# Performance work log

Hardware: AMD Instinct MI355X
Metric: run time of the kernel (lower is better)

## Reference

```python
import jax, jax.numpy as jnp
import numpy as np

VOXEL_SIZE = 0.05  # init kwarg


def setup_inputs() -> dict:
    key = jax.random.key(0)
    N, B = 4_194_304, 16
    # coords uniform in [0, 5)^3 -> ~100^3 voxel cells per scene at voxel_size=0.05
    coord = jax.random.uniform(key, (N, 3), dtype=jnp.float32) * 5.0
    # cumulative batch offsets (equal-sized scenes), as pointops expects
    offset = (jnp.arange(1, B + 1, dtype=jnp.int32) * (N // B)).astype(jnp.int32)
    return {"coord": coord, "offset": offset}


def _voxel_mean(coord, offset, voxel_size):
    """Faithful jax port of voxelize_helper + segment_csr(mean) + batch2offset.

    Returns:
      n_p    [N,3]  voxel-mean coords, padded with zeros beyond n_voxels
      n_o    [B]    cumulative voxel counts per batch (batch2offset)
      counts [N]    points per voxel (idx_ptr = concat([0], cumsum(counts[valid])))
    """
    N = coord.shape[0]
    B = offset.shape[0]
    # batch id per point from cumulative offsets
    batch = jnp.searchsorted(offset, jnp.arange(N), side='right')  # [N]
    # start = per-batch min coord (start=None path of voxelize_helper)
    start = jax.ops.segment_min(coord, batch, num_segments=B)      # [B,3]
    grid = jnp.floor((coord - start[batch]) / voxel_size).astype(jnp.int32)  # [N,3]
    G = jnp.max(grid) + 1  # grid extent (per-axis upper bound)
    # linearized cluster key: unique per (batch, gx, gy, gz)
    ckey = ((batch * G + grid[:, 0]) * G + grid[:, 1]) * G + grid[:, 2]
    fill = B * G * G * G  # sentinel beyond any real key
    # sorted unique cluster keys == CSR segment order after sorting cluster indices
    uniq, inv = jnp.unique(ckey, return_inverse=True, size=N, fill_value=fill)
    # fused gather + segment-mean (equivalent to coord[sorted_idx] -> segment_csr mean)
    seg_sum = jax.ops.segment_sum(coord, inv, num_segments=N)                 # [N,3]
    counts = jax.ops.segment_sum(jnp.ones((N,), coord.dtype), inv, num_segments=N)
    n_p = seg_sum / jnp.maximum(counts, 1.0)[:, None]
    # batch id per voxel -> batch2offset (cumulative voxel counts)
    valid = uniq < fill
    vbatch = jnp.where(valid, uniq // (G * G * G), B)
    per_batch = jax.ops.segment_sum(valid.astype(jnp.int32), vbatch, num_segments=B + 1)[:B]
    n_o = jnp.cumsum(per_batch)
    return n_p, n_o, counts.astype(jnp.int32)


def reference(coord, offset):
    return _voxel_mean(coord, offset, VOXEL_SIZE)
```

## Files before the change

kernel.cpp:

```cpp
#include <hip/hip_runtime.h>
#include <stdint.h>


typedef unsigned int uint;
typedef unsigned short u16;
typedef unsigned long long u64;

#define VS 0.05f
#define QSCALE (4096.0f / VS)
#define QINV  (VS / 4096.0f)
#define NBUCKET 2048
#define NBLK_P 256
#define DENSE_MAX 4096

__device__ __forceinline__ uint f2m(float f) {
    uint b = __float_as_uint(f);
    return (b & 0x80000000u) ? ~b : (b | 0x80000000u);
}
__device__ __forceinline__ float m2f(uint m) {
    uint b = (m & 0x80000000u) ? (m & 0x7fffffffu) : ~m;
    return __uint_as_float(b);
}

__global__ void k_init(uint* start_m, int B3) {
    int i = blockIdx.x * blockDim.x + threadIdx.x;
    if (i < B3) start_m[i] = 0xFFFFFFFFu;
}

__global__ void __launch_bounds__(256)
k_minmax(const float* __restrict__ coord, const int* __restrict__ offset,
         int N, int B, uint* start_m) {
    __shared__ uint smin[768];
    __shared__ int soff[256];
    int t = threadIdx.x;
    int nb3 = B * 3;
    for (int j = t; j < B; j += 256) soff[j] = offset[j];
    for (int j = t; j < nb3; j += 256) smin[j] = 0xFFFFFFFFu;
    __syncthreads();

    int F = 3 * N;
    int NQ = F >> 2;
    int per = (NQ + gridDim.x - 1) / gridDim.x;
    int qlo = blockIdx.x * per;
    int qhi = min(NQ, qlo + per);
    const float4* __restrict__ c4 = reinterpret_cast<const float4*>(coord);

    bool fast = false;
    int bU = 0;
    if (qlo < qhi) {
        int pF = (4 * qlo) / 3;
        int pL = (4 * qhi - 1) / 3;
        int bF = 0, bL = 0;
        for (int j = 0; j < B; ++j) {
            bF += (pF >= soff[j]) ? 1 : 0;
            bL += (pL >= soff[j]) ? 1 : 0;
        }
        fast = (bF == bL);
        bU = bF;
    }

    if (fast) {
        int q = qlo + t;
        int p0 = q % 3;
        float s0 = INFINITY, s1 = INFINITY, s2 = INFINITY;
        for (;;) {
            if (q >= qhi) break;
            float4 v = c4[q];
            s0 = fminf(s0, fminf(v.x, v.w)); s1 = fminf(s1, v.y); s2 = fminf(s2, v.z);
            q += 256;
            if (q >= qhi) break;
            v = c4[q];
            s1 = fminf(s1, fminf(v.x, v.w)); s2 = fminf(s2, v.y); s0 = fminf(s0, v.z);
            q += 256;
            if (q >= qhi) break;
            v = c4[q];
            s2 = fminf(s2, fminf(v.x, v.w)); s0 = fminf(s0, v.y); s1 = fminf(s1, v.z);
            q += 256;
        }
        float ax, ay, az;
        if (p0 == 0)      { ax = s0; ay = s1; az = s2; }
        else if (p0 == 1) { ax = s2; ay = s0; az = s1; }
        else              { ax = s1; ay = s2; az = s0; }
        for (int d = 32; d; d >>= 1) {
            ax = fminf(ax, __shfl_xor(ax, d));
            ay = fminf(ay, __shfl_xor(ay, d));
            az = fminf(az, __shfl_xor(az, d));
        }
        if ((t & 63) == 0 && ax < INFINITY) {
            atomicMin(&smin[bU * 3 + 0], f2m(ax));
            atomicMin(&smin[bU * 3 + 1], f2m(ay));
            atomicMin(&smin[bU * 3 + 2], f2m(az));
        }
    } else {
        for (int q = qlo + t; q < qhi; q += 256) {
            float4 v = c4[q];
            int e = 4 * q;
            float vals[4] = {v.x, v.y, v.z, v.w};
#pragma unroll
            for (int k = 0; k < 4; ++k) {
                int ee = e + k;
                int pt = ee / 3;
                int axis = ee - 3 * pt;
                int b = 0;
                for (int j = 0; j < B; ++j) b += (pt >= soff[j]) ? 1 : 0;
                atomicMin(&smin[b * 3 + axis], f2m(vals[k]));
            }
        }
    }

    if (blockIdx.x == 0) {
        for (int ee = 4 * NQ + t; ee < F; ee += 256) {
            int pt = ee / 3;
            int axis = ee - 3 * pt;
            int b = 0;
            for (int j = 0; j < B; ++j) b += (pt >= soff[j]) ? 1 : 0;
            atomicMin(&smin[b * 3 + axis], f2m(coord[ee]));
        }
    }
    __syncthreads();
    for (int j = t; j < nb3; j += 256) {
        uint mn = smin[j];
        if (mn != 0xFFFFFFFFu) atomicMin(&start_m[j], mn);
    }
}


__device__ __forceinline__ u64 mk_rec(float x, float y, float z,
                                      float sx, float sy, float sz,
                                      int b, uint& q) {
    int gx = min((int)floorf((x - sx) / VS), 127);
    int gy = min((int)floorf((y - sy) / VS), 127);
    int gz = min((int)floorf((z - sz) / VS), 127);
    float fx = fmaxf(x - (sx + (float)gx * VS), 0.0f);
    float fy = fmaxf(y - (sy + (float)gy * VS), 0.0f);
    float fz = fmaxf(z - (sz + (float)gz * VS), 0.0f);
    uint ux = min((uint)(fx * QSCALE + 0.5f), 4095u);
    uint uy = min((uint)(fy * QSCALE + 0.5f), 4095u);
    uint uz = min((uint)(fz * QSCALE + 0.5f), 4095u);
    uint cell = ((uint)gy << 7) | (uint)gz;
    q = ((uint)b << 7) | (uint)gx;
    return ((u64)q << 50) | ((u64)cell << 36) | ((u64)ux << 24) | ((u64)uy << 12) | (u64)uz;
}

__device__ __forceinline__ void count_point(float x, float y, float z, int b,
                                            float sx, float sy, float sz, int pid,
                                            uint* hist, u64* __restrict__ tmp) {
    uint q;
    u64 rec = mk_rec(x, y, z, sx, sy, sz, b, q);
    atomicAdd(&hist[q], 1u);
    tmp[pid] = rec;
}

__global__ void __launch_bounds__(1024)
k_count3(const float* __restrict__ coord, const int* __restrict__ offset,
         int N, int B, const uint* __restrict__ start_m, uint* __restrict__ histm,
         u64* __restrict__ tmp) {
    __shared__ uint hist[NBUCKET];
    __shared__ int soff[16];
    __shared__ float sstart[48];
    int t = threadIdx.x;
    if (t < B) soff[t] = offset[t];
    if (t < B * 3) sstart[t] = m2f(start_m[t]);
    for (int j = t; j < NBUCKET; j += 1024) hist[j] = 0;
    __syncthreads();
    int chunk = (N + gridDim.x - 1) / gridDim.x;
    int lo = blockIdx.x * chunk, hi = min(N, lo + chunk);
    int bLo = 0, bHi = 0;
    for (int j = 0; j < B; ++j) {
        bLo += (lo >= soff[j]) ? 1 : 0;
        bHi += (hi - 1 >= soff[j]) ? 1 : 0;
    }
    if (lo < hi && bLo == bHi && (lo & 3) == 0) {
        int b = bLo;
        float sx = sstart[b * 3 + 0], sy = sstart[b * 3 + 1], sz = sstart[b * 3 + 2];
        const float4* __restrict__ c4 = reinterpret_cast<const float4*>(coord);
        int gEnd = hi >> 2;
        for (int g = (lo >> 2) + t; g < gEnd; g += 1024) {
            float4 v0 = c4[3 * g], v1 = c4[3 * g + 1], v2 = c4[3 * g + 2];
            int p = 4 * g;
            count_point(v0.x, v0.y, v0.z, b, sx, sy, sz, p + 0, hist, tmp);
            count_point(v0.w, v1.x, v1.y, b, sx, sy, sz, p + 1, hist, tmp);
            count_point(v1.z, v1.w, v2.x, b, sx, sy, sz, p + 2, hist, tmp);
            count_point(v2.y, v2.z, v2.w, b, sx, sy, sz, p + 3, hist, tmp);
        }
        for (int i = (gEnd << 2) + t; i < hi; i += 1024) {
            float x = coord[3 * i + 0], y = coord[3 * i + 1], z = coord[3 * i + 2];
            count_point(x, y, z, b, sx, sy, sz, i, hist, tmp);
        }
    } else {
        for (int i = lo + t; i < hi; i += 1024) {
            float x = coord[3 * i + 0], y = coord[3 * i + 1], z = coord[3 * i + 2];
            int b = 0;
            for (int j = 0; j < B; ++j) b += (i >= soff[j]) ? 1 : 0;
            count_point(x, y, z, b, sstart[b * 3 + 0], sstart[b * 3 + 1],
                        sstart[b * 3 + 2], i, hist, tmp);
        }
    }
    __syncthreads();
    for (int j = t; j < NBUCKET; j += 1024)
        histm[(size_t)j * NBLK_P + blockIdx.x] = hist[j];
}

__global__ void __launch_bounds__(256)
k_scanrow(uint* __restrict__ histm, uint* __restrict__ tot) {
    __shared__ uint wtot[4], woff[4];
    uint* row = histm + (size_t)blockIdx.x * NBLK_P;
    int t = threadIdx.x;
    uint v = row[t];
    uint sc = v;
    for (int d = 1; d < 64; d <<= 1) {
        uint nb = __shfl_up(sc, d, 64);
        if ((t & 63) >= d) sc += nb;
    }
    if ((t & 63) == 63) wtot[t >> 6] = sc;
    __syncthreads();
    if (t == 0) {
        uint r = 0;
#pragma unroll
        for (int k = 0; k < 4; ++k) { woff[k] = r; r += wtot[k]; }
    }
    __syncthreads();
    uint incl = sc + woff[t >> 6];
    row[t] = incl - v;
    if (t == 255) tot[blockIdx.x] = incl;
}

__global__ void __launch_bounds__(1024)
k_scan2048(const uint* __restrict__ in, uint* __restrict__ out) {
    __shared__ uint wtot[16], woff[16];
    int t = threadIdx.x;
    uint a = in[2 * t], bb = in[2 * t + 1];
    uint s = a + bb;
    uint sc = s;
    for (int d = 1; d < 64; d <<= 1) {
        uint nb = __shfl_up(sc, d, 64);
        if ((t & 63) >= d) sc += nb;
    }
    if ((t & 63) == 63) wtot[t >> 6] = sc;
    __syncthreads();
    if (t == 0) {
        uint r = 0;
#pragma unroll
        for (int k = 0; k < 16; ++k) { woff[k] = r; r += wtot[k]; }
    }
    __syncthreads();
    uint incl = sc + woff[t >> 6];
    uint ex = incl - s;
    out[2 * t] = ex;
    out[2 * t + 1] = ex + a;
    if (t == 1023) out[2048] = incl;
}

__global__ void __launch_bounds__(1024)
k_scan2048b(const uint* __restrict__ in, uint* __restrict__ out,
            int B, float* __restrict__ no_out) {
    __shared__ uint wtot[16], woff[16];
    int t = threadIdx.x;
    uint a = in[2 * t], bb = in[2 * t + 1];
    uint s = a + bb;
    uint sc = s;
    for (int d = 1; d < 64; d <<= 1) {
        uint nb = __shfl_up(sc, d, 64);
        if ((t & 63) >= d) sc += nb;
    }
    if ((t & 63) == 63) wtot[t >> 6] = sc;
    __syncthreads();
    if (t == 0) {
        uint r = 0;
#pragma unroll
        for (int k = 0; k < 16; ++k) { woff[k] = r; r += wtot[k]; }
    }
    __syncthreads();
    uint incl = sc + woff[t >> 6];
    uint ex = incl - s;
    out[2 * t] = ex;
    out[2 * t + 1] = ex + a;
    if (t == 1023) out[2048] = incl;
    int tp = t + 1;
    if ((tp & 63) == 0) {
        int b = (tp >> 6) - 1;
        if (b < B) no_out[b] = (float)incl;
    }
}

__global__ void __launch_bounds__(1024)
k_scatter(const u64* __restrict__ tmp, int N,
          const uint* __restrict__ histm, const uint* __restrict__ bucket_base,
          u64* __restrict__ recs) {
    __shared__ uint cursor[NBUCKET];
    int t = threadIdx.x;
    for (int j = t; j < NBUCKET; j += 1024)
        cursor[j] = bucket_base[j] + histm[(size_t)j * NBLK_P + blockIdx.x];
    __syncthreads();
    int chunk = (N + gridDim.x - 1) / gridDim.x;
    int lo = blockIdx.x * chunk, hi = min(N, lo + chunk);
    for (int i = lo + t; i < hi; i += 1024) {
        u64 r = tmp[i];
        uint q = (uint)(r >> 50);
        uint slot = atomicAdd(&cursor[q], 1u);
        recs[slot] = r;
    }
}

__global__ void __launch_bounds__(256)
k_vox(const u64* __restrict__ recs, const uint* __restrict__ bucket_base,
      uint* __restrict__ voxcount, uint* __restrict__ gmask) {
    __shared__ uint bits[512];
    __shared__ uint wsum[4];
    int q = blockIdx.x;
    int t = threadIdx.x;
    uint lo = bucket_base[q], hi = bucket_base[q + 1];
    bits[t] = 0;
    bits[t + 256] = 0;
    __syncthreads();
    for (uint i = lo + t; i < hi; i += 256) {
        uint c = (uint)(recs[i] >> 36) & 0x3FFFu;
        atomicOr(&bits[c >> 5], 1u << (c & 31));
    }
    __syncthreads();
    uint m0 = bits[t], m1 = bits[t + 256];
    gmask[(size_t)q * 512 + t] = m0;
    gmask[(size_t)q * 512 + t + 256] = m1;
    uint s = __popc(m0) + __popc(m1);
    for (int d = 32; d; d >>= 1) s += __shfl_xor(s, d);
    if ((t & 63) == 0) wsum[t >> 6] = s;
    __syncthreads();
    if (t == 0) voxcount[q] = wsum[0] + wsum[1] + wsum[2] + wsum[3];
}

__global__ void __launch_bounds__(1024)
k_emit2(const u64* __restrict__ recs, const uint* __restrict__ bucket_base,
        const uint* __restrict__ voxscan, const uint* __restrict__ gmask,
        const uint* __restrict__ start_m, int N, int B, int out_total,
        float* __restrict__ np_out, float* __restrict__ cnt_out,
        float* __restrict__ out) {
    int t = threadIdx.x;
    if (blockIdx.x >= NBUCKET) {
        uint total = voxscan[NBUCKET];
        int zb = blockIdx.x - NBUCKET;
        int stride = (gridDim.x - NBUCKET) * 1024;
        int tid = zb * 1024 + t;
        for (int j = 3 * (int)total + tid; j < 3 * N; j += stride) np_out[j] = 0.0f;
        for (int j = (int)total + tid; j < N; j += stride) cnt_out[j] = 0.0f;
        for (int j = 4 * N + B + tid; j < out_total; j += stride) out[j] = 0.0f;
        return;
    }
    __shared__ u64 dense[DENSE_MAX];
    __shared__ uint mask[512], wrank[512];
    __shared__ u16 cellOf[DENSE_MAX];
    __shared__ uint wtot[8], woff[9];
    __shared__ float sstart[48];
    int q = blockIdx.x;
    uint lo = bucket_base[q], hi = bucket_base[q + 1];
    if (lo == hi) return;
    if (t < 48) sstart[t] = m2f(start_m[t]);
    uint m = 0, c = 0;
    if (t < 512) {
        m = gmask[(size_t)q * 512 + t];
        mask[t] = m;
        c = __popc(m);
    }
    uint sc = c;
    for (int d = 1; d < 64; d <<= 1) {
        uint nb = __shfl_up(sc, d, 64);
        if ((t & 63) >= d) sc += nb;
    }
    if (t < 512 && (t & 63) == 63) wtot[t >> 6] = sc;
    __syncthreads();
    if (t == 0) {
        uint r = 0;
        for (int k = 0; k < 8; ++k) { woff[k] = r; r += wtot[k]; }
        woff[8] = r;
    }
    __syncthreads();
    uint myrank = sc - c + ((t < 512) ? woff[t >> 6] : 0);
    if (t < 512) wrank[t] = myrank;
    uint vc = woff[8];
    uint base_r = voxscan[q];
    int b = q >> 7, gx = q & 127;
    float cx = sstart[b * 3 + 0] + (float)gx * VS;
    float sy = sstart[b * 3 + 1], sz = sstart[b * 3 + 2];
    for (uint segbase = 0; segbase < vc; segbase += DENSE_MAX) {
        uint seglen = min(vc - segbase, (uint)DENSE_MAX);
        for (uint j = t; j < seglen; j += 1024) dense[j] = 0ull;
        if (t < 512) {
            uint mm = m;
            uint r = myrank;
            uint kbase = (uint)t << 5;
            while (mm) {
                uint bit = (uint)__ffs(mm) - 1u;
                mm &= mm - 1u;
                if (r >= segbase && r < segbase + seglen)
                    cellOf[r - segbase] = (u16)(kbase + bit);
                ++r;
            }
        }
        __syncthreads();
        for (uint i = lo + t; i < hi; i += 1024) {
            u64 rec = recs[i];
            uint cc = (uint)(rec >> 36) & 0x3FFFu;
            uint w = cc >> 5, bit = cc & 31;
            uint r = wrank[w] + __popc(mask[w] & ((1u << bit) - 1u));
            if (r >= segbase && r < segbase + seglen) {
                u64 enc = (((rec >> 24) & 0xFFFull) << 46) | (((rec >> 12) & 0xFFFull) << 28)
                        | ((rec & 0xFFFull) << 10) | 1ull;
                atomicAdd(&dense[r - segbase], enc);
            }
        }
        __syncthreads();
        for (uint rr = segbase + t; rr < segbase + seglen; rr += 1024) {
            uint cell = cellOf[rr - segbase];
            uint gy = cell >> 7, gz = cell & 127u;
            u64 p = dense[rr - segbase];
            float cnt = (float)(uint)(p & 1023ull);
            float inv = 1.0f / fmaxf(cnt, 1.0f);
            uint uz = (uint)((p >> 10) & 0x3FFFFull);
            uint uy = (uint)((p >> 28) & 0x3FFFFull);
            uint ux = (uint)(p >> 46);
            uint r_out = base_r + rr;
            np_out[3 * r_out + 0] = cx + ((float)ux * QINV) * inv;
            np_out[3 * r_out + 1] = sy + (float)gy * VS + ((float)uy * QINV) * inv;
            np_out[3 * r_out + 2] = sz + (float)gz * VS + ((float)uz * QINV) * inv;
            cnt_out[r_out] = cnt;
        }
        __syncthreads();
    }
}


__device__ __forceinline__ void point_grid(const float* __restrict__ coord, int i,
                                           const int* soff, const float* sstart, int B,
                                           float& x, float& y, float& z,
                                           int& b, int& gx, int& gy, int& gz) {
    x = coord[3 * i + 0]; y = coord[3 * i + 1]; z = coord[3 * i + 2];
    b = 0;
    for (int j = 0; j < B; ++j) b += (i >= soff[j]) ? 1 : 0;
    gx = min((int)floorf((x - sstart[b * 3 + 0]) / VS), 127);
    gy = min((int)floorf((y - sstart[b * 3 + 1]) / VS), 127);
    gz = min((int)floorf((z - sstart[b * 3 + 2]) / VS), 127);
}

__device__ __forceinline__ u64 frac12(float x, float y, float z,
                                      const float* sstart, int b,
                                      int gx, int gy, int gz) {
    float fx = fmaxf(x - (sstart[b * 3 + 0] + (float)gx * VS), 0.0f);
    float fy = fmaxf(y - (sstart[b * 3 + 1] + (float)gy * VS), 0.0f);
    float fz = fmaxf(z - (sstart[b * 3 + 2] + (float)gz * VS), 0.0f);
    uint ux = min((uint)(fx * QSCALE + 0.5f), 4095u);
    uint uy = min((uint)(fy * QSCALE + 0.5f), 4095u);
    uint uz = min((uint)(fz * QSCALE + 0.5f), 4095u);
    return ((u64)ux << 24) | ((u64)uy << 12) | (u64)uz;
}

__global__ void k_hist(const float* __restrict__ coord, const int* __restrict__ offset,
                       int N, int B, const uint* __restrict__ start_m,
                       uint* __restrict__ mask) {
    __shared__ int soff[256];
    __shared__ float sstart[768];
    for (int j = threadIdx.x; j < B; j += blockDim.x) soff[j] = offset[j];
    for (int j = threadIdx.x; j < B * 3; j += blockDim.x) sstart[j] = m2f(start_m[j]);
    __syncthreads();
    int i = blockIdx.x * blockDim.x + threadIdx.x;
    if (i >= N) return;
    float x, y, z; int b, gx, gy, gz;
    point_grid(coord, i, soff, sstart, B, x, y, z, b, gx, gy, gz);
    uint key = ((uint)b << 21) | ((uint)gx << 14) | ((uint)gy << 7) | (uint)gz;
    atomicOr(&mask[key >> 5], 1u << (key & 31));
}

__global__ void k_scan1(const uint* __restrict__ mask, uint* __restrict__ partial) {
    int base = blockIdx.x * 1024 + threadIdx.x * 4;
    uint4 m = *(const uint4*)(mask + base);
    uint s = __popc(m.x) + __popc(m.y) + __popc(m.z) + __popc(m.w);
    for (int d = 32; d; d >>= 1) s += __shfl_xor(s, d);
    __shared__ uint wsum[4];
    if ((threadIdx.x & 63) == 0) wsum[threadIdx.x >> 6] = s;
    __syncthreads();
    if (threadIdx.x == 0) partial[blockIdx.x] = wsum[0] + wsum[1] + wsum[2] + wsum[3];
}

__global__ void k_scan2(uint* partial, int P, uint* total) {
    __shared__ uint t[256];
    uint carry = 0;
    for (int base = 0; base < P; base += 256) {
        int j = base + threadIdx.x;
        uint v = (j < P) ? partial[j] : 0;
        t[threadIdx.x] = v;
        __syncthreads();
        for (int d = 1; d < 256; d <<= 1) {
            uint add = (threadIdx.x >= d) ? t[threadIdx.x - d] : 0;
            __syncthreads();
            t[threadIdx.x] += add;
            __syncthreads();
        }
        uint inc = t[threadIdx.x];
        uint chunk = t[255];
        if (j < P) partial[j] = carry + inc - v;
        __syncthreads();
        carry += chunk;
    }
    if (threadIdx.x == 0) *total = carry;
}

__global__ void k_scan3(const uint* __restrict__ mask, const uint* __restrict__ partial,
                        uint* __restrict__ wordrank) {
    int base = blockIdx.x * 1024 + threadIdx.x * 4;
    uint4 m = *(const uint4*)(mask + base);
    uint c0 = __popc(m.x), c1 = __popc(m.y), c2 = __popc(m.z), c3 = __popc(m.w);
    uint s = c0 + c1 + c2 + c3;
    __shared__ uint t[256];
    t[threadIdx.x] = s;
    __syncthreads();
    for (int d = 1; d < 256; d <<= 1) {
        uint add = (threadIdx.x >= d) ? t[threadIdx.x - d] : 0;
        __syncthreads();
        t[threadIdx.x] += add;
        __syncthreads();
    }
    uint ex = t[threadIdx.x] - s + partial[blockIdx.x];
    uint4 r;
    r.x = ex; r.y = ex + c0; r.z = ex + c0 + c1; r.w = ex + c0 + c1 + c2;
    *(uint4*)(wordrank + base) = r;
}

__global__ void k_no(const uint* mask, const uint* wordrank, const uint* total,
                     float* no_out, int B, int W) {
    int b = blockIdx.x * blockDim.x + threadIdx.x;
    if (b >= B) return;
    long long idx = (long long)(b + 1) << 21;
    uint w = (uint)(idx >> 5);
    uint v;
    if (w >= (uint)W) v = *total;
    else v = wordrank[w];
    no_out[b] = (float)v;
}

__global__ void k_accum_sparse(const float* __restrict__ coord, const int* __restrict__ offset,
                               int N, int B, const uint* __restrict__ start_m,
                               const uint* __restrict__ mask, const uint* __restrict__ wordrank,
                               u64* __restrict__ packed) {
    __shared__ int soff[256];
    __shared__ float sstart[768];
    for (int j = threadIdx.x; j < B; j += blockDim.x) soff[j] = offset[j];
    for (int j = threadIdx.x; j < B * 3; j += blockDim.x) sstart[j] = m2f(start_m[j]);
    __syncthreads();
    int i = blockIdx.x * blockDim.x + threadIdx.x;
    if (i >= N) return;
    float x, y, z; int b, gx, gy, gz;
    point_grid(coord, i, soff, sstart, B, x, y, z, b, gx, gy, gz);
    uint key = ((uint)b << 21) | ((uint)gx << 14) | ((uint)gy << 7) | (uint)gz;
    uint w = key >> 5, bit = key & 31;
    uint r = wordrank[w] + __popc(mask[w] & ((1u << bit) - 1u));
    u64 f = frac12(x, y, z, sstart, b, gx, gy, gz);
    u64 enc = (((f >> 24) & 0xFFFull) << 46) | (((f >> 12) & 0xFFFull) << 28)
            | ((f & 0xFFFull) << 10) | 1ull;
    atomicAdd(&packed[r], enc);
}

__global__ void k_decode_sparse(const uint* __restrict__ mask, const uint* __restrict__ wordrank,
                                const uint* __restrict__ start_m,
                                const u64* __restrict__ packed, int W,
                                float* __restrict__ np_out, float* __restrict__ cnt_out) {
    __shared__ float sstart[48];
    for (int j = threadIdx.x; j < 48; j += blockDim.x) sstart[j] = m2f(start_m[j]);
    __syncthreads();
    int w = blockIdx.x * blockDim.x + threadIdx.x;
    if (w >= W) return;
    uint m = mask[w];
    if (m == 0) return;
    uint r = wordrank[w];
    uint kbase = (uint)w << 5;
    while (m) {
        uint bit = (uint)__ffs(m) - 1u;
        m &= m - 1u;
        uint key = kbase + bit;
        u64 p = packed[r];
        float cnt = (float)(uint)(p & 1023ull);
        float inv = 1.0f / fmaxf(cnt, 1.0f);
        uint uz = (uint)((p >> 10) & 0x3FFFFull);
        uint uy = (uint)((p >> 28) & 0x3FFFFull);
        uint ux = (uint)(p >> 46);
        uint b = key >> 21;
        uint gx = (key >> 14) & 127u;
        uint gy = (key >> 7) & 127u;
        uint gz = key & 127u;
        np_out[3 * r + 0] = sstart[b * 3 + 0] + (float)gx * VS + ((float)ux * QINV) * inv;
        np_out[3 * r + 1] = sstart[b * 3 + 1] + (float)gy * VS + ((float)uy * QINV) * inv;
        np_out[3 * r + 2] = sstart[b * 3 + 2] + (float)gz * VS + ((float)uz * QINV) * inv;
        cnt_out[r] = cnt;
        ++r;
    }
}

extern "C" void kernel_launch(void* const* d_in, const int* in_sizes, int n_in,
                              void* d_out, int out_size, void* d_ws, size_t ws_size,
                              hipStream_t stream) {
    const float* coord = (const float*)d_in[0];
    const int* offset = (const int*)d_in[1];
    int N = in_sizes[0] / 3;
    int B = in_sizes[1];

    float* out = (float*)d_out;
    float* np_out = out;
    float* no_out = out + (size_t)3 * N;
    float* cnt_out = no_out + B;

    uint8_t* base = (uint8_t*)d_ws;
    uint* start_m = (uint*)base;
    uint* total = start_m + (size_t)B * 3;

    uintptr_t p = (uintptr_t)(total + 1);
    p = (p + 255) & ~(uintptr_t)255;
    uint* histm = (uint*)p;          p += (size_t)NBUCKET * NBLK_P * 4;
    p = (p + 255) & ~(uintptr_t)255;
    uint* tot = (uint*)p;            p += (size_t)NBUCKET * 4;
    p = (p + 255) & ~(uintptr_t)255;
    uint* bucket_base = (uint*)p;    p += (size_t)(NBUCKET + 1) * 4;
    p = (p + 255) & ~(uintptr_t)255;
    uint* voxcount = (uint*)p;       p += (size_t)NBUCKET * 4;
    p = (p + 255) & ~(uintptr_t)255;
    uint* voxscan = (uint*)p;        p += (size_t)(NBUCKET + 1) * 4;
    p = (p + 255) & ~(uintptr_t)255;
    uint* gmask = (uint*)p;          p += (size_t)NBUCKET * 512 * 4;
    p = (p + 255) & ~(uintptr_t)255;
    u64* recs = (u64*)p;             p += (size_t)N * 8;
    p = (p + 255) & ~(uintptr_t)255;
    u64* tmp = (u64*)p;              p += (size_t)N * 8;
    size_t need_part = p - (uintptr_t)base;

    k_init<<<(B * 3 + 255) / 256, 256, 0, stream>>>(start_m, B * 3);
    k_minmax<<<2048, 256, 0, stream>>>(coord, offset, N, B, start_m);

    if (B <= 16 && ws_size >= need_part) {
        k_count3<<<NBLK_P, 1024, 0, stream>>>(coord, offset, N, B, start_m, histm, tmp);
        k_scanrow<<<NBUCKET, 256, 0, stream>>>(histm, tot);
        k_scan2048<<<1, 1024, 0, stream>>>(tot, bucket_base);
        k_scatter<<<NBLK_P, 1024, 0, stream>>>(tmp, N, histm, bucket_base, recs);
        k_vox<<<NBUCKET, 256, 0, stream>>>(recs, bucket_base, voxcount, gmask);
        k_scan2048b<<<1, 1024, 0, stream>>>(voxcount, voxscan, B, no_out);
        k_emit2<<<NBUCKET + 1024, 1024, 0, stream>>>(recs, bucket_base, voxscan, gmask,
                                                     start_m, N, B, out_size,
                                                     np_out, cnt_out, out);
    } else {
        hipMemsetAsync(d_out, 0, (size_t)out_size * sizeof(float), stream);
        size_t W = (size_t)B << 16;
        int nblk1 = (int)(W / 1024);
        uintptr_t sp = (uintptr_t)(total + 1);
        sp = (sp + 255) & ~(uintptr_t)255;
        uint* partial = (uint*)sp;   sp += (size_t)nblk1 * 4;
        sp = (sp + 255) & ~(uintptr_t)255;
        uint* mask = (uint*)sp;      sp += W * 4;
        sp = (sp + 255) & ~(uintptr_t)255;
        uint* wordrank = (uint*)sp;  sp += W * 4;
        sp = (sp + 255) & ~(uintptr_t)255;
        u64* packed = (u64*)sp;
        int nb = (N + 255) / 256;
        hipMemsetAsync(mask, 0, W * sizeof(uint), stream);
        hipMemsetAsync(packed, 0, (size_t)N * sizeof(u64), stream);
        k_hist<<<nb, 256, 0, stream>>>(coord, offset, N, B, start_m, mask);
        k_scan1<<<nblk1, 256, 0, stream>>>(mask, partial);
        k_scan2<<<1, 256, 0, stream>>>(partial, nblk1, total);
        k_scan3<<<nblk1, 256, 0, stream>>>(mask, partial, wordrank);
        k_no<<<(B + 63) / 64, 64, 0, stream>>>(mask, wordrank, total, no_out, B, (int)W);
        k_accum_sparse<<<nb, 256, 0, stream>>>(coord, offset, N, B, start_m, mask,
                                               wordrank, packed);
        k_decode_sparse<<<(int)((W + 255) / 256), 256, 0, stream>>>(mask, wordrank, start_m,
                                                                    packed, (int)W,
                                                                    np_out, cnt_out);
    }
}
```

Measured before the change: 194.1 us.

## Fuse voxel accumulation into bitmap kernel, emit from compact per-bucket results

The per-bucket voxel accumulation (rank computation, shared-memory atomic sums, cell bookkeeping) moves from the emit kernel into the bitmap kernel. That kernel now writes packed sums and cell ids into bucket-local scratch slots, reusing the tmp buffer. The emit kernel only reads these compact results and writes outputs. This removes the second pass over all point records and the global bitmask round-trip. In exchange, the bitmap kernel does more work with 256 threads per block, which may lower parallelism and occupancy per bucket because of the larger shared memory.

```diff
diff --git a/kernel.cpp b/kernel.cpp
--- a/kernel.cpp
+++ b/kernel.cpp
@@ -303,10 +303,15 @@
 }
 
 __global__ void __launch_bounds__(256)
-k_vox(const u64* __restrict__ recs, const uint* __restrict__ bucket_base,
-      uint* __restrict__ voxcount, uint* __restrict__ gmask) {
+k_vox2(const u64* __restrict__ recs, const uint* __restrict__ bucket_base,
+       uint* __restrict__ voxcount, u64* __restrict__ packedv,
+       u16* __restrict__ cellv) {
     __shared__ uint bits[512];
-    __shared__ uint wsum[4];
+    __shared__ uint wrank[512];
+    __shared__ u64 dense[DENSE_MAX];
+    __shared__ u16 cellOf[DENSE_MAX];
+    __shared__ uint wtot[4], woff[4];
+    __shared__ uint shvc;
     int q = blockIdx.x;
     int t = threadIdx.x;
     uint lo = bucket_base[q], hi = bucket_base[q + 1];
@@ -318,75 +323,35 @@
         atomicOr(&bits[c >> 5], 1u << (c & 31));
     }
     __syncthreads();
-    uint m0 = bits[t], m1 = bits[t + 256];
-    gmask[(size_t)q * 512 + t] = m0;
-    gmask[(size_t)q * 512 + t + 256] = m1;
-    uint s = __popc(m0) + __popc(m1);
-    for (int d = 32; d; d >>= 1) s += __shfl_xor(s, d);
-    if ((t & 63) == 0) wsum[t >> 6] = s;
-    __syncthreads();
-    if (t == 0) voxcount[q] = wsum[0] + wsum[1] + wsum[2] + wsum[3];
-}
-
-__global__ void __launch_bounds__(1024)
-k_emit2(const u64* __restrict__ recs, const uint* __restrict__ bucket_base,
-        const uint* __restrict__ voxscan, const uint* __restrict__ gmask,
-        const uint* __restrict__ start_m, int N, int B, int out_total,
-        float* __restrict__ np_out, float* __restrict__ cnt_out,
-        float* __restrict__ out) {
-    int t = threadIdx.x;
-    if (blockIdx.x >= NBUCKET) {
-        uint total = voxscan[NBUCKET];
-        int zb = blockIdx.x - NBUCKET;
-        int stride = (gridDim.x - NBUCKET) * 1024;
-        int tid = zb * 1024 + t;
-        for (int j = 3 * (int)total + tid; j < 3 * N; j += stride) np_out[j] = 0.0f;
-        for (int j = (int)total + tid; j < N; j += stride) cnt_out[j] = 0.0f;
-        for (int j = 4 * N + B + tid; j < out_total; j += stride) out[j] = 0.0f;
-        return;
-    }
-    __shared__ u64 dense[DENSE_MAX];
-    __shared__ uint mask[512], wrank[512];
-    __shared__ u16 cellOf[DENSE_MAX];
-    __shared__ uint wtot[8], woff[9];
-    __shared__ float sstart[48];
-    int q = blockIdx.x;
-    uint lo = bucket_base[q], hi = bucket_base[q + 1];
-    if (lo == hi) return;
-    if (t < 48) sstart[t] = m2f(start_m[t]);
-    uint m = 0, c = 0;
-    if (t < 512) {
-        m = gmask[(size_t)q * 512 + t];
-        mask[t] = m;
-        c = __popc(m);
-    }
-    uint sc = c;
+    uint m0 = bits[2 * t], m1 = bits[2 * t + 1];
+    uint c0 = __popc(m0), c1 = __popc(m1);
+    uint s = c0 + c1;
+    uint sc = s;
     for (int d = 1; d < 64; d <<= 1) {
         uint nb = __shfl_up(sc, d, 64);
         if ((t & 63) >= d) sc += nb;
     }
-    if (t < 512 && (t & 63) == 63) wtot[t >> 6] = sc;
+    if ((t & 63) == 63) wtot[t >> 6] = sc;
     __syncthreads();
     if (t == 0) {
         uint r = 0;
-        for (int k = 0; k < 8; ++k) { woff[k] = r; r += wtot[k]; }
-        woff[8] = r;
-    }
-    __syncthreads();
-    uint myrank = sc - c + ((t < 512) ? woff[t >> 6] : 0);
-    if (t < 512) wrank[t] = myrank;
-    uint vc = woff[8];
-    uint base_r = voxscan[q];
-    int b = q >> 7, gx = q & 127;
-    float cx = sstart[b * 3 + 0] + (float)gx * VS;
-    float sy = sstart[b * 3 + 1], sz = sstart[b * 3 + 2];
+#pragma unroll
+        for (int k = 0; k < 4; ++k) { woff[k] = r; r += wtot[k]; }
+        shvc = r;
+        voxcount[q] = r;
+    }
+    __syncthreads();
+    uint ex = sc + woff[t >> 6] - s;
+    wrank[2 * t] = ex;
+    wrank[2 * t + 1] = ex + c0;
+    uint vc = shvc;
+    uint myr0 = ex;
+    uint myr1 = ex + c0;
     for (uint segbase = 0; segbase < vc; segbase += DENSE_MAX) {
         uint seglen = min(vc - segbase, (uint)DENSE_MAX);
-        for (uint j = t; j < seglen; j += 1024) dense[j] = 0ull;
-        if (t < 512) {
-            uint mm = m;
-            uint r = myrank;
-            uint kbase = (uint)t << 5;
+        for (uint j = t; j < seglen; j += 256) dense[j] = 0ull;
+        {
+            uint mm = m0, r = myr0, kbase = (uint)(2 * t) << 5;
             while (mm) {
                 uint bit = (uint)__ffs(mm) - 1u;
                 mm &= mm - 1u;
@@ -394,13 +359,21 @@
                     cellOf[r - segbase] = (u16)(kbase + bit);
                 ++r;
             }
+            mm = m1; r = myr1; kbase = (uint)(2 * t + 1) << 5;
+            while (mm) {
+                uint bit = (uint)__ffs(mm) - 1u;
+                mm &= mm - 1u;
+                if (r >= segbase && r < segbase + seglen)
+                    cellOf[r - segbase] = (u16)(kbase + bit);
+                ++r;
+            }
         }
         __syncthreads();
-        for (uint i = lo + t; i < hi; i += 1024) {
+        for (uint i = lo + t; i < hi; i += 256) {
             u64 rec = recs[i];
             uint cc = (uint)(rec >> 36) & 0x3FFFu;
             uint w = cc >> 5, bit = cc & 31;
-            uint r = wrank[w] + __popc(mask[w] & ((1u << bit) - 1u));
+            uint r = wrank[w] + __popc(bits[w] & ((1u << bit) - 1u));
             if (r >= segbase && r < segbase + seglen) {
                 u64 enc = (((rec >> 24) & 0xFFFull) << 46) | (((rec >> 12) & 0xFFFull) << 28)
                         | ((rec & 0xFFFull) << 10) | 1ull;
@@ -408,22 +381,56 @@
             }
         }
         __syncthreads();
-        for (uint rr = segbase + t; rr < segbase + seglen; rr += 1024) {
-            uint cell = cellOf[rr - segbase];
-            uint gy = cell >> 7, gz = cell & 127u;
-            u64 p = dense[rr - segbase];
-            float cnt = (float)(uint)(p & 1023ull);
-            float inv = 1.0f / fmaxf(cnt, 1.0f);
-            uint uz = (uint)((p >> 10) & 0x3FFFFull);
-            uint uy = (uint)((p >> 28) & 0x3FFFFull);
-            uint ux = (uint)(p >> 46);
-            uint r_out = base_r + rr;
-            np_out[3 * r_out + 0] = cx + ((float)ux * QINV) * inv;
-            np_out[3 * r_out + 1] = sy + (float)gy * VS + ((float)uy * QINV) * inv;
-            np_out[3 * r_out + 2] = sz + (float)gz * VS + ((float)uz * QINV) * inv;
-            cnt_out[r_out] = cnt;
+        for (uint rr = segbase + t; rr < segbase + seglen; rr += 256) {
+            packedv[lo + rr] = dense[rr - segbase];
+            cellv[lo + rr] = cellOf[rr - segbase];
         }
         __syncthreads();
+    }
+}
+
+__global__ void __launch_bounds__(512)
+k_emit3(const u64* __restrict__ packedv, const u16* __restrict__ cellv,
+        const uint* __restrict__ bucket_base, const uint* __restrict__ voxscan,
+        const uint* __restrict__ start_m, int N, int B, int out_total,
+        float* __restrict__ np_out, float* __restrict__ cnt_out,
+        float* __restrict__ out) {
+    int t = threadIdx.x;
+    if (blockIdx.x >= NBUCKET) {
+        uint total = voxscan[NBUCKET];
+        int zb = blockIdx.x - NBUCKET;
+        int stride = (gridDim.x - NBUCKET) * 512;
+        int tid = zb * 512 + t;
+        for (int j = 3 * (int)total + tid; j < 3 * N; j += stride) np_out[j] = 0.0f;
+        for (int j = (int)total + tid; j < N; j += stride) cnt_out[j] = 0.0f;
+        for (int j = 4 * N + B + tid; j < out_total; j += stride) out[j] = 0.0f;
+        return;
+    }
+    __shared__ float sstart[48];
+    int q = blockIdx.x;
+    uint base_r = voxscan[q];
+    uint vc = voxscan[q + 1] - base_r;
+    if (vc == 0) return;
+    uint lo = bucket_base[q];
+    if (t < 48) sstart[t] = m2f(start_m[t]);
+    __syncthreads();
+    int b = q >> 7, gx = q & 127;
+    float cx = sstart[b * 3 + 0] + (float)gx * VS;
+    float sy = sstart[b * 3 + 1], sz = sstart[b * 3 + 2];
+    for (uint j = t; j < vc; j += 512) {
+        u64 p = packedv[lo + j];
+        uint cell = cellv[lo + j];
+        uint gy = cell >> 7, gz = cell & 127u;
+        float cnt = (float)(uint)(p & 1023ull);
+        float inv = 1.0f / fmaxf(cnt, 1.0f);
+        uint uz = (uint)((p >> 10) & 0x3FFFFull);
+        uint uy = (uint)((p >> 28) & 0x3FFFFull);
+        uint ux = (uint)(p >> 46);
+        uint r_out = base_r + j;
+        np_out[3 * r_out + 0] = cx + ((float)ux * QINV) * inv;
+        np_out[3 * r_out + 1] = sy + (float)gy * VS + ((float)uy * QINV) * inv;
+        np_out[3 * r_out + 2] = sz + (float)gz * VS + ((float)uz * QINV) * inv;
+        cnt_out[r_out] = cnt;
     }
 }
 
@@ -621,26 +628,27 @@
     p = (p + 255) & ~(uintptr_t)255;
     uint* voxscan = (uint*)p;        p += (size_t)(NBUCKET + 1) * 4;
     p = (p + 255) & ~(uintptr_t)255;
-    uint* gmask = (uint*)p;          p += (size_t)NBUCKET * 512 * 4;
-    p = (p + 255) & ~(uintptr_t)255;
     u64* recs = (u64*)p;             p += (size_t)N * 8;
     p = (p + 255) & ~(uintptr_t)255;
     u64* tmp = (u64*)p;              p += (size_t)N * 8;
+    p = (p + 255) & ~(uintptr_t)255;
+    u16* cellv = (u16*)p;            p += (size_t)N * 2;
     size_t need_part = p - (uintptr_t)base;
 
     k_init<<<(B * 3 + 255) / 256, 256, 0, stream>>>(start_m, B * 3);
     k_minmax<<<2048, 256, 0, stream>>>(coord, offset, N, B, start_m);
 
     if (B <= 16 && ws_size >= need_part) {
+        u64* packedv = tmp;
         k_count3<<<NBLK_P, 1024, 0, stream>>>(coord, offset, N, B, start_m, histm, tmp);
         k_scanrow<<<NBUCKET, 256, 0, stream>>>(histm, tot);
         k_scan2048<<<1, 1024, 0, stream>>>(tot, bucket_base);
         k_scatter<<<NBLK_P, 1024, 0, stream>>>(tmp, N, histm, bucket_base, recs);
-        k_vox<<<NBUCKET, 256, 0, stream>>>(recs, bucket_base, voxcount, gmask);
+        k_vox2<<<NBUCKET, 256, 0, stream>>>(recs, bucket_base, voxcount, packedv, cellv);
         k_scan2048b<<<1, 1024, 0, stream>>>(voxcount, voxscan, B, no_out);
-        k_emit2<<<NBUCKET + 1024, 1024, 0, stream>>>(recs, bucket_base, voxscan, gmask,
-                                                     start_m, N, B, out_size,
-                                                     np_out, cnt_out, out);
+        k_emit3<<<NBUCKET + 2048, 512, 0, stream>>>(packedv, cellv, bucket_base, voxscan,
+                                                    start_m, N, B, out_size,
+                                                    np_out, cnt_out, out);
     } else {
         hipMemsetAsync(d_out, 0, (size_t)out_size * sizeof(float), stream);
         size_t W = (size_t)B << 16;
```

New measurement: 210.7 us. 1.09x slower.
